# Performance work log

Hardware: AMD Instinct MI355X
Metric: run time of the kernel (lower is better)

The kernel has to match this reference:

```python
import jax, jax.numpy as jnp
import numpy as np

DIM = 4096
N_HEADS = 32
HEAD_DIM = DIM // N_HEADS
BSZ = 4
SEQLEN = 512
MAX_SEQ = 2048
NEG = -1e9


def _qlinear(x, q, s):
    # int-quantized weight [out,in] dequantized with per-output-channel scale
    w = q.astype(jnp.float32) * s[:, None]
    return jnp.einsum('bsd,od->bso', x, w)


def _apply_rotary(xq, xk, cos, sin):
    # xq,xk: [b,s,h,hd]; cos,sin: [s,hd/2]
    def rot(t):
        b, s, h, d = t.shape
        t = t.reshape(b, s, h, d // 2, 2)
        tr, ti = t[..., 0], t[..., 1]
        c = cos[None, :, None, :]
        sn = sin[None, :, None, :]
        out_r = tr * c - ti * sn
        out_i = tr * sn + ti * c
        return jnp.stack([out_r, out_i], axis=-1).reshape(b, s, h, d)
    return rot(xq), rot(xk)


def setup_inputs() -> dict:
    key = jax.random.key(0)
    ks = jax.random.split(key, 12)
    x = jax.random.normal(ks[0], (BSZ, SEQLEN, DIM), dtype=jnp.float32)
    inv = 1.0 / (10000.0 ** (jnp.arange(0, HEAD_DIM, 2, dtype=jnp.float32) / HEAD_DIM))
    ang = jnp.arange(SEQLEN, dtype=jnp.float32)[:, None] * inv[None, :]
    freqs_cos, freqs_sin = jnp.cos(ang), jnp.sin(ang)
    input_idexes = jnp.arange(SEQLEN, dtype=jnp.int32)  # cache slots being written
    # causal additive mask over full cache: query at position i may attend j <= i
    j = jnp.arange(MAX_SEQ)
    mask = jnp.where(j[None, :] <= input_idexes[:, None], 0.0, NEG).astype(jnp.float32)
    mask = mask[None, None]  # [1,1,S,MAX_SEQ]
    cache_k = jnp.zeros((BSZ, MAX_SEQ, N_HEADS, HEAD_DIM), jnp.float32)
    cache_v = jnp.zeros((BSZ, MAX_SEQ, N_HEADS, HEAD_DIM), jnp.float32)
    SCALE = 2.0 / (127.0 * np.sqrt(DIM))
    def mkw(kq, kscale):
        q = jax.random.randint(kq, (DIM, DIM), -127, 128, dtype=jnp.int32)
        s = jax.random.uniform(kscale, (DIM,), dtype=jnp.float32) * SCALE
        return q, s
    wq_q, wq_s = mkw(ks[1], ks[2])
    wk_q, wk_s = mkw(ks[3], ks[4])
    wv_q, wv_s = mkw(ks[5], ks[6])
    wo_q, wo_s = mkw(ks[7], ks[8])
    return dict(x=x, freqs_cos=freqs_cos, freqs_sin=freqs_sin, mask=mask,
                input_idexes=input_idexes, cache_k=cache_k, cache_v=cache_v,
                wq_q=wq_q, wq_s=wq_s, wk_q=wk_q, wk_s=wk_s,
                wv_q=wv_q, wv_s=wv_s, wo_q=wo_q, wo_s=wo_s)


def reference(x, freqs_cos, freqs_sin, mask, input_idexes, cache_k, cache_v,
              wq_q, wq_s, wk_q, wk_s, wv_q, wv_s, wo_q, wo_s):
    bsz, seqlen, _ = x.shape
    xq = _qlinear(x, wq_q, wq_s).reshape(bsz, seqlen, N_HEADS, HEAD_DIM)
    xk = _qlinear(x, wk_q, wk_s).reshape(bsz, seqlen, N_HEADS, HEAD_DIM)
    xv = _qlinear(x, wv_q, wv_s).reshape(bsz, seqlen, N_HEADS, HEAD_DIM)
    xq, xk = _apply_rotary(xq, xk, freqs_cos, freqs_sin)
    # KV-cache append (index_copy on dim 1)
    cache_k = cache_k.at[:, input_idexes].set(xk)
    cache_v = cache_v.at[:, input_idexes].set(xv)
    # [b,h,q,d] x [b,h,k,d] -> [b,h,q,k]
    scores = jnp.einsum('bqhd,bkhd->bhqk', xq, cache_k) / np.sqrt(HEAD_DIM)
    scores = scores + mask
    probs = jax.nn.softmax(scores.astype(jnp.float32), axis=-1).astype(xq.dtype)
    out = jnp.einsum('bhqk,bkhd->bqhd', probs, cache_v).reshape(bsz, seqlen, -1)
    out = _qlinear(out, wo_q, wo_s)
    return out, (cache_k, cache_v)
```

## Files before the change

kernel.cpp:

```cpp
#include <hip/hip_runtime.h>
#include <cstdint>
#include <cstddef>

typedef __bf16 bf16;
typedef __attribute__((ext_vector_type(8))) __bf16 bf16x8;
typedef __attribute__((ext_vector_type(2))) __bf16 bf16x2;
typedef __attribute__((ext_vector_type(4))) float f32x4;
typedef __attribute__((ext_vector_type(2))) float f32x2;
typedef __attribute__((ext_vector_type(4))) int i32x4;

#define DIMN 4096
#define SEQ 512
#define MAXSEQ 2048
#define NHEAD 32
#define HD 128

#define BM 128
#define BN 128
#define BK 32

__device__ __forceinline__ void gld_lds16(const void* g, void* l) {
  __builtin_amdgcn_global_load_lds(
      (const __attribute__((address_space(1))) unsigned int*)g,
      (__attribute__((address_space(3))) unsigned int*)l, 16, 0, 0);
}

__device__ __forceinline__ void gemm_core(const bf16* Ablk, const bf16* Bblk,
                                          int lda, int ldb, int kmax,
                                          f32x4 acc[4][4], bf16* As, bf16* Bs) {
  const int tid = threadIdx.x;
  const int wave = tid >> 6;
  const int lane = tid & 63;
  const int wm = (wave >> 1) * 64;
  const int wn = (wave & 1) * 64;
  const int lrow = lane & 15;
  const int lkq8 = (lane >> 4) * 8;
  const int srow = wave * 32 + (lane >> 2);
  const int scol = (lane & 3) * 8;
  const bf16* Ag = Ablk + (size_t)srow * lda + scol;
  const bf16* Bg = Bblk + (size_t)srow * ldb + scol;
  bf16* lA = As + wave * 32 * BK;
  bf16* lB = Bs + wave * 32 * BK;

  for (int k0 = 0; k0 < kmax; k0 += BK) {
    __syncthreads();
    gld_lds16(Ag + k0, lA);
    gld_lds16(Ag + k0 + (size_t)16 * lda, lA + 16 * BK);
    gld_lds16(Bg + k0, lB);
    gld_lds16(Bg + k0 + (size_t)16 * ldb, lB + 16 * BK);
    __syncthreads();
    bf16x8 a[4], b[4];
#pragma unroll
    for (int i = 0; i < 4; ++i)
      a[i] = *(const bf16x8*)(As + (wm + i * 16 + lrow) * BK + lkq8);
#pragma unroll
    for (int i = 0; i < 4; ++i)
      b[i] = *(const bf16x8*)(Bs + (wn + i * 16 + lrow) * BK + lkq8);
#pragma unroll
    for (int mi = 0; mi < 4; ++mi)
#pragma unroll
      for (int ni = 0; ni < 4; ++ni)
        acc[mi][ni] = __builtin_amdgcn_mfma_f32_16x16x32_bf16(a[mi], b[ni], acc[mi][ni], 0, 0, 0);
  }
}


#define PBAR do {                              \
    asm volatile("" ::: "memory");             \
    __builtin_amdgcn_sched_barrier(0);         \
    __builtin_amdgcn_s_barrier();              \
    __builtin_amdgcn_sched_barrier(0);         \
    asm volatile("" ::: "memory");             \
  } while (0)

#define STG_A(KT, C, LB) \
  gld_lds16(Asrc + (KT) * 128 + (size_t)(C) * 64 * DIMN, (LB) + (C) * 8192 + sdst)
#define STG_B(KT, C, LB) \
  gld_lds16(Bsrc + (KT) * 128 + (size_t)(C) * 64 * DIMN, (LB) + 16384 + (C) * 8192 + sdst)

#define LDA8(DST, MI, H, LB) \
  DST = *(const i32x4*)((LB) + (MI) * 2048 + aoff + ((H) ? g1off : g0off))
#define LDB8(DST, NI, H, LB) \
  DST = *(const i32x4*)((LB) + 16384 + (NI) * 2048 + boff + ((H) ? g1off : g0off))

#define MFMA16I()                                                           \
    __builtin_amdgcn_s_setprio(1);                                          \
    _Pragma("unroll") for (int _i = 0; _i < 4; ++_i)                        \
      _Pragma("unroll") for (int _n = 0; _n < 4; ++_n)                      \
        acc[_i][_n] = __builtin_amdgcn_mfma_i32_16x16x64_i8(                \
            a[_i], b[_n], acc[_i][_n], 0, 0, 0);                            \
    __builtin_amdgcn_s_setprio(0)

#define TILE3(T, CUR, STG) do {                                             \
    i32x4 a[4], b[4];                                                       \
                         \
    _Pragma("unroll") for (int n = 0; n < 4; ++n) LDB8(b[n], n, 0, CUR);    \
    _Pragma("unroll") for (int i = 0; i < 4; ++i) LDA8(a[i], i, 0, CUR);    \
    STG_B((T) + 2, 0, STG);                                                 \
    STG_B((T) + 2, 1, STG);                                                 \
    STG_A((T) + 2, 0, STG);                                                 \
    MFMA16I();                                                              \
                        \
    _Pragma("unroll") for (int n = 0; n < 4; ++n) LDB8(b[n], n, 1, CUR);    \
    _Pragma("unroll") for (int i = 0; i < 4; ++i) LDA8(a[i], i, 1, CUR);    \
    STG_B((T) + 2, 2, STG);                                                 \
    STG_B((T) + 2, 3, STG);                                                 \
    STG_A((T) + 2, 1, STG);                                                 \
    MFMA16I();                                                              \
                                   \
    asm volatile("s_waitcnt vmcnt(6)" ::: "memory");                        \
    __builtin_amdgcn_sched_barrier(0);                                      \
    __builtin_amdgcn_s_barrier();                                           \
    __builtin_amdgcn_sched_barrier(0);                                      \
  } while (0)

__device__ __forceinline__ void gemm128x256_i8(const char* __restrict__ Ablk,
                                               const char* __restrict__ Bblk,
                                               char* lds, i32x4 acc[4][4]) {
  const int tid = threadIdx.x;
  const int wave = tid >> 6, lane = tid & 63;
  const int wm = (wave >> 2) * 64, wn = (wave & 3) * 64;
  const int lrow = lane & 15, q = lane >> 4;
  const int qx = q ^ (lrow & 3);
  const int hbit = (lrow >> 2) & 1;
  const int g0off = (((hbit) << 2) | qx) << 4;
  const int g1off = (((hbit ^ 1) << 2) | qx) << 4;
  const int aoff = (wm + lrow) * 128;
  const int boff = (wn + lrow) * 128;
  const int gsw = ((lane & 7) ^ (lane >> 3)) << 4;
  const char* Asrc = Ablk + (size_t)(wave * 8 + (lane >> 3)) * DIMN + gsw;
  const char* Bsrc = Bblk + (size_t)(wave * 8 + (lane >> 3)) * DIMN + gsw;
  const int sdst = wave * 1024;
  char* const L0 = lds;
  char* const L1 = lds + 49152;
  char* const L2 = lds + 98304;

  STG_A(0, 0, L0); STG_A(0, 1, L0);
  STG_B(0, 0, L0); STG_B(0, 1, L0); STG_B(0, 2, L0); STG_B(0, 3, L0);
  STG_A(1, 0, L1); STG_A(1, 1, L1);
  STG_B(1, 0, L1); STG_B(1, 1, L1); STG_B(1, 2, L1); STG_B(1, 3, L1);
  asm volatile("s_waitcnt vmcnt(6)" ::: "memory");
  __builtin_amdgcn_sched_barrier(0);
  __builtin_amdgcn_s_barrier();
  __builtin_amdgcn_sched_barrier(0);

  for (int t = 0; t < 30; t += 3) {
    TILE3(t, L0, L2);
    TILE3(t + 1, L1, L0);
    TILE3(t + 2, L2, L1);
  }
  TILE3(30, L0, L2);
  TILE3(31, L1, L0);
}

#define ACC_INIT_F(acc)                                 \
  f32x4 acc[4][4];                                      \
  _Pragma("unroll") for (int _i = 0; _i < 4; ++_i)      \
      _Pragma("unroll") for (int _j = 0; _j < 4; ++_j)  \
          acc[_i][_j] = f32x4{0.f, 0.f, 0.f, 0.f};

#define ACC_INIT_I8(acc)                                \
  i32x4 acc[4][4];                                      \
  _Pragma("unroll") for (int _i = 0; _i < 4; ++_i)      \
      _Pragma("unroll") for (int _j = 0; _j < 4; ++_j)  \
          acc[_i][_j] = i32x4{0, 0, 0, 0};

#define EPI_COORDS                                      \
  const int lane = threadIdx.x & 63;                    \
  const int wave = threadIdx.x >> 6;                    \
  const int wm = (wave >> 1) * 64, wn = (wave & 1) * 64;\
  const int cq = (lane >> 4) * 4, cc = lane & 15;

#define EPI8_COORDS                                      \
  const int lane = threadIdx.x & 63;                     \
  const int wave = threadIdx.x >> 6;                     \
  const int wm = (wave >> 2) * 64, wn = (wave & 3) * 64; \
  const int cq = (lane >> 4) * 4, cc = lane & 15;

__global__ __launch_bounds__(256) void k_prep(
    const int* __restrict__ q0, const int* __restrict__ q1,
    const int* __restrict__ q2, const int* __restrict__ q3,
    char* __restrict__ w8, const float* __restrict__ x,
    char* __restrict__ x8, float* __restrict__ xs,
    float* __restrict__ ck, float* __restrict__ cv) {
  __shared__ float red[4];
  const int bx = blockIdx.x;
  const int tid = threadIdx.x;
  if (bx < 16384) {
    const int w = bx >> 12;
    const int* q = (w == 0) ? q0 : (w == 1) ? q1 : (w == 2) ? q2 : q3;
    char* wp = w8 + (size_t)w * 16777216ull;
    size_t i = ((size_t)(bx & 4095) * 256 + tid) * 16;
    const i32x4* qp = (const i32x4*)(q + i);
    i32x4 a = qp[0], b = qp[1], c = qp[2], d = qp[3];
    i32x4 o;
    o[0] = (a[0] & 255) | ((a[1] & 255) << 8) | ((a[2] & 255) << 16) | (a[3] << 24);
    o[1] = (b[0] & 255) | ((b[1] & 255) << 8) | ((b[2] & 255) << 16) | (b[3] << 24);
    o[2] = (c[0] & 255) | ((c[1] & 255) << 8) | ((c[2] & 255) << 16) | (c[3] << 24);
    o[3] = (d[0] & 255) | ((d[1] & 255) << 8) | ((d[2] & 255) << 16) | (d[3] << 24);
    *(i32x4*)(wp + i) = o;
  } else if (bx < 18432) {
    const int row = bx - 16384;
    const float* src = x + (size_t)row * DIMN + tid * 16;
    f32x4 v[4];
#pragma unroll
    for (int j = 0; j < 4; ++j) v[j] = ((const f32x4*)src)[j];
    float am = 0.f;
#pragma unroll
    for (int j = 0; j < 4; ++j)
#pragma unroll
      for (int e = 0; e < 4; ++e) am = fmaxf(am, fabsf(v[j][e]));
#pragma unroll
    for (int off = 32; off; off >>= 1) am = fmaxf(am, __shfl_xor(am, off, 64));
    if ((tid & 63) == 0) red[tid >> 6] = am;
    __syncthreads();
    am = fmaxf(fmaxf(red[0], red[1]), fmaxf(red[2], red[3]));
    const float inv = am > 0.f ? 127.f / am : 0.f;
    i32x4 o;
#pragma unroll
    for (int j = 0; j < 4; ++j) {
      int b0 = (int)rintf(v[j][0] * inv), b1 = (int)rintf(v[j][1] * inv);
      int b2 = (int)rintf(v[j][2] * inv), b3 = (int)rintf(v[j][3] * inv);
      o[j] = (b0 & 255) | ((b1 & 255) << 8) | ((b2 & 255) << 16) | (b3 << 24);
    }
    *(i32x4*)(x8 + (size_t)row * DIMN + tid * 16) = o;
    if (tid == 0) xs[row] = am * (1.f / 127.f);
  } else {
    const int z = bx - 18432;
    const int region = z / 6144;
    const int zoff = z - region * 6144;
    const int b = region >> 1;
    float* base = (region & 1) ? cv : ck;
    char* p = (char*)(base + ((size_t)b * MAXSEQ + SEQ) * DIMN);
    *(f32x4*)(p + (size_t)zoff * 4096 + tid * 16) = f32x4{0.f, 0.f, 0.f, 0.f};
  }
}

__global__ __launch_bounds__(256) void k_quant_attn(const bf16* __restrict__ at,
                                                    char* __restrict__ a8,
                                                    float* __restrict__ as_) {
  __shared__ float red[4];
  const int row = blockIdx.x, tid = threadIdx.x;
  const bf16* src = at + (size_t)row * DIMN + tid * 16;
  bf16x8 h0 = ((const bf16x8*)src)[0], h1 = ((const bf16x8*)src)[1];
  float f[16];
#pragma unroll
  for (int j = 0; j < 8; ++j) { f[j] = (float)h0[j]; f[8 + j] = (float)h1[j]; }
  float am = 0.f;
#pragma unroll
  for (int j = 0; j < 16; ++j) am = fmaxf(am, fabsf(f[j]));
#pragma unroll
  for (int off = 32; off; off >>= 1) am = fmaxf(am, __shfl_xor(am, off, 64));
  if ((tid & 63) == 0) red[tid >> 6] = am;
  __syncthreads();
  am = fmaxf(fmaxf(red[0], red[1]), fmaxf(red[2], red[3]));
  const float inv = am > 0.f ? 127.f / am : 0.f;
  i32x4 o;
#pragma unroll
  for (int j = 0; j < 4; ++j) {
    int b0 = (int)rintf(f[j * 4 + 0] * inv), b1 = (int)rintf(f[j * 4 + 1] * inv);
    int b2 = (int)rintf(f[j * 4 + 2] * inv), b3 = (int)rintf(f[j * 4 + 3] * inv);
    o[j] = (b0 & 255) | ((b1 & 255) << 8) | ((b2 & 255) << 16) | (b3 << 24);
  }
  *(i32x4*)(a8 + (size_t)row * DIMN + tid * 16) = o;
  if (tid == 0) as_[row] = am * (1.f / 127.f);
}

__global__ __launch_bounds__(512, 2) void k_gemm_qkv8(
    const char* __restrict__ X8, const char* __restrict__ W8,
    const float* __restrict__ xs, const float* __restrict__ sq,
    const float* __restrict__ sk, const float* __restrict__ sv,
    const float* __restrict__ fc, const float* __restrict__ fs,
    const int* __restrict__ idx, bf16* __restrict__ qbf,
    bf16* __restrict__ kbf, float* __restrict__ ck, float* __restrict__ cv) {
  __shared__ __align__(16) char lds[147456];
  const int n0 = blockIdx.x * 256;
  const int m0 = blockIdx.y * 128;
  const int z = blockIdx.z;
  const char* W = W8 + (size_t)z * 16777216ull;
  const float* sw = (z == 0) ? sq : (z == 1) ? sk : sv;
  ACC_INIT_I8(acc);
  gemm128x256_i8(X8 + (size_t)m0 * DIMN, W + (size_t)n0 * DIMN, lds, acc);
  EPI8_COORDS;
  if (z < 2) {
    bf16* dst = (z == 0) ? qbf : kbf;
#pragma unroll
    for (int mi = 0; mi < 4; ++mi)
#pragma unroll
      for (int ni = 0; ni < 4; ++ni)
#pragma unroll
        for (int r = 0; r < 4; ++r) {
          const int row = m0 + wm + mi * 16 + cq + r;
          const int col = n0 + wn + ni * 16 + cc;
          const float v = (float)acc[mi][ni][r] * xs[row] * sw[col];
          const float pv = __shfl_xor(v, 1, 64);
          const int s = row & 511, b = row >> 9;
          const int hd = col & 127, h = col >> 7;
          const int d2 = hd >> 1;
          const float c = fc[s * 64 + d2], sn = fs[s * 64 + d2];
          const float o = (col & 1) ? (pv * sn + v * c) : (v * c - pv * sn);
          dst[(((size_t)(b * NHEAD + h)) * SEQ + s) * HD + hd] = (bf16)o;
          if (z == 1) {
            const int pos = idx[s];
            ck[((size_t)b * MAXSEQ + pos) * DIMN + col] = o;
          }
        }
  } else {
#pragma unroll
    for (int mi = 0; mi < 4; ++mi)
#pragma unroll
      for (int ni = 0; ni < 4; ++ni)
#pragma unroll
        for (int r = 0; r < 4; ++r) {
          const int row = m0 + wm + mi * 16 + cq + r;
          const int col = n0 + wn + ni * 16 + cc;
          const int s = row & 511, b = row >> 9;
          cv[((size_t)b * MAXSEQ + s) * DIMN + col] =
              (float)acc[mi][ni][r] * xs[row] * sw[col];
        }
  }
}

__global__ __launch_bounds__(256) void k_vt(const float* __restrict__ cv,
                                            bf16* __restrict__ vt) {
  __shared__ float tile[32][129];
  const int s0 = blockIdx.x * 32;
  const int bh = blockIdx.y;
  const int b = bh >> 5, h = bh & 31;
  const int tid = threadIdx.x;
  const float* src = cv + (size_t)b * MAXSEQ * DIMN + h * HD;
#pragma unroll
  for (int p = 0; p < 16; ++p) {
    const int row = p * 2 + (tid >> 7);
    const int d = tid & 127;
    tile[row][d] = src[(size_t)(s0 + row) * DIMN + d];
  }
  __syncthreads();
  bf16* dst = vt + (size_t)bh * HD * SEQ;
#pragma unroll
  for (int c = 0; c < 16; ++c) {
    const int d = c * 8 + (tid >> 5);
    const int sl = tid & 31;
    dst[(size_t)d * SEQ + s0 + sl] = (bf16)tile[sl][d];
  }
}

__constant__ int g_tm[10] = {0, 1, 1, 2, 2, 2, 3, 3, 3, 3};
__constant__ int g_tn[10] = {0, 0, 1, 0, 1, 2, 0, 1, 2, 3};

__global__ __launch_bounds__(256, 2) void k_gemm_qk(
    const bf16* __restrict__ qb, const bf16* __restrict__ kb,
    bf16* __restrict__ sc) {
  const int m0 = g_tm[blockIdx.x] * BM;
  const int n0 = g_tn[blockIdx.x] * BN;
  const int bh = blockIdx.z;
  __shared__ __align__(16) bf16 As[BM * BK];
  __shared__ __align__(16) bf16 Bs[BN * BK];
  ACC_INIT_F(acc);
  gemm_core(qb + (size_t)bh * SEQ * HD + (size_t)m0 * HD,
            kb + (size_t)bh * SEQ * HD + (size_t)n0 * HD, HD, HD, HD, acc, As, Bs);
  EPI_COORDS;
  bf16* dst = sc + (size_t)bh * SEQ * SEQ;
#pragma unroll
  for (int mi = 0; mi < 4; ++mi)
#pragma unroll
    for (int ni = 0; ni < 4; ++ni)
#pragma unroll
      for (int r = 0; r < 4; ++r) {
        const int row = m0 + wm + mi * 16 + cq + r;
        const int col = n0 + wn + ni * 16 + cc;
        dst[(size_t)row * SEQ + col] = (bf16)(acc[mi][ni][r] * 0.08838834764831845f);
      }
}

__global__ __launch_bounds__(256) void k_softmax(bf16* __restrict__ sc) {
  const int row = blockIdx.x * 4 + (threadIdx.x >> 6);
  const int lane = threadIdx.x & 63;
  const int q = row & 511;
  bf16* p = sc + (size_t)row * SEQ + lane * 8;
  bf16x8 v8 = *(const bf16x8*)p;
  float lv[8];
  float m = -3.0e38f;
#pragma unroll
  for (int j = 0; j < 8; ++j) {
    const int kj = lane * 8 + j;
    lv[j] = (kj <= q) ? (float)v8[j] : -3.0e38f;
    m = fmaxf(m, lv[j]);
  }
#pragma unroll
  for (int off = 32; off; off >>= 1) m = fmaxf(m, __shfl_xor(m, off, 64));
  float e[8];
  float sum = 0.f;
#pragma unroll
  for (int j = 0; j < 8; ++j) {
    e[j] = (lane * 8 + j <= q) ? __expf(lv[j] - m) : 0.f;
    sum += e[j];
  }
#pragma unroll
  for (int off = 32; off; off >>= 1) sum += __shfl_xor(sum, off, 64);
  const float r = 1.f / sum;
  bf16x8 o;
#pragma unroll
  for (int j = 0; j < 8; ++j) o[j] = (bf16)(e[j] * r);
  *(bf16x8*)p = o;
}

__global__ __launch_bounds__(256, 2) void k_gemm_pv(
    const bf16* __restrict__ P, const bf16* __restrict__ vt,
    bf16* __restrict__ attn) {
  const int m0 = blockIdx.y * BM;
  const int bh = blockIdx.z;
  const int kmax = m0 + BM;
  __shared__ __align__(16) bf16 As[BM * BK];
  __shared__ __align__(16) bf16 Bs[BN * BK];
  ACC_INIT_F(acc);
  gemm_core(P + (size_t)bh * SEQ * SEQ + (size_t)m0 * SEQ,
            vt + (size_t)bh * HD * SEQ, SEQ, SEQ, kmax, acc, As, Bs);
  EPI_COORDS;
  const int b = bh >> 5, h = bh & 31;
#pragma unroll
  for (int mi = 0; mi < 4; ++mi)
#pragma unroll
    for (int ni = 0; ni < 4; ++ni)
#pragma unroll
      for (int r = 0; r < 4; ++r) {
        const int row = m0 + wm + mi * 16 + cq + r;
        const int col = wn + ni * 16 + cc;
        attn[((size_t)(b * SEQ + row)) * DIMN + h * HD + col] = (bf16)acc[mi][ni][r];
      }
}

__global__ __launch_bounds__(512, 2) void k_gemm_out8(
    const char* __restrict__ A8, const char* __restrict__ WO8,
    const float* __restrict__ as_, const float* __restrict__ so,
    float* __restrict__ out) {
  __shared__ __align__(16) char lds[147456];
  const int n0 = blockIdx.x * 256;
  const int m0 = blockIdx.y * 128;
  ACC_INIT_I8(acc);
  gemm128x256_i8(A8 + (size_t)m0 * DIMN, WO8 + (size_t)n0 * DIMN, lds, acc);
  EPI8_COORDS;
#pragma unroll
  for (int mi = 0; mi < 4; ++mi)
#pragma unroll
    for (int ni = 0; ni < 4; ++ni)
#pragma unroll
      for (int r = 0; r < 4; ++r) {
        const int row = m0 + wm + mi * 16 + cq + r;
        const int col = n0 + wn + ni * 16 + cc;
        out[(size_t)row * DIMN + col] = (float)acc[mi][ni][r] * as_[row] * so[col];
      }
}

extern "C" void kernel_launch(void* const* d_in, const int* in_sizes, int n_in,
                              void* d_out, int out_size, void* d_ws, size_t ws_size,
                              hipStream_t stream) {
  const float* x = (const float*)d_in[0];
  const float* fc = (const float*)d_in[1];
  const float* fs = (const float*)d_in[2];
  const int* idx = (const int*)d_in[4];
  const int* wq_q = (const int*)d_in[7];
  const int* wk_q = (const int*)d_in[9];
  const int* wv_q = (const int*)d_in[11];
  const int* wo_q = (const int*)d_in[13];
  const float* wq_s = (const float*)d_in[8];
  const float* wk_s = (const float*)d_in[10];
  const float* wv_s = (const float*)d_in[12];
  const float* wo_s = (const float*)d_in[14];

  float* out = (float*)d_out;
  float* ck_out = out + 8388608;
  float* cv_out = ck_out + 33554432;

  char* ws = (char*)d_ws;
  char* W8   = ws;
  char* X8   = ws + 67108864ull;
  float* XS  = (float*)(ws + 75497472ull);
  float* AS  = (float*)(ws + 75513856ull);
  bf16* QBF  = (bf16*)(ws + 83886080ull);
  bf16* KBF  = (bf16*)(ws + 100663296ull);
  bf16* VTB  = (bf16*)(ws + 117440512ull);
  bf16* ATTN = (bf16*)(ws + 134217728ull);
  char* A8   = ws + 150994944ull;
  bf16* SC   = (bf16*)(ws + 167772160ull);

  k_prep<<<dim3(67584), 256, 0, stream>>>(wq_q, wk_q, wv_q, wo_q, W8, x, X8, XS,
                                          ck_out, cv_out);
  k_gemm_qkv8<<<dim3(16, 16, 3), 512, 0, stream>>>(
      X8, W8, XS, wq_s, wk_s, wv_s, fc, fs, idx, QBF, KBF, ck_out, cv_out);
  k_vt<<<dim3(16, 128), 256, 0, stream>>>(cv_out, VTB);
  k_gemm_qk<<<dim3(10, 1, 128), 256, 0, stream>>>(QBF, KBF, SC);
  k_softmax<<<dim3(16384), 256, 0, stream>>>(SC);
  k_gemm_pv<<<dim3(1, 4, 128), 256, 0, stream>>>(SC, VTB, ATTN);
  k_quant_attn<<<dim3(2048), 256, 0, stream>>>(ATTN, A8, AS);
  k_gemm_out8<<<dim3(16, 16), 512, 0, stream>>>(A8, W8 + 50331648ull, AS, wo_s, out);
  (void)in_sizes; (void)n_in; (void)out_size; (void)ws_size;
}
```

Baseline: 857.0 us.

## Move KV-cache tail zeroing from prep kernel into QKV GEMM main loop

The prep kernel no longer zeroes the unused tail of the KV caches. Instead, each QKV GEMM block writes a slice of zeros once per K-loop iteration, interleaved with the MFMA pipeline. The goal is to hide this write-only memory traffic, about 200MB, behind the compute-bound int8 GEMM and to shrink the prep launch. In exchange it adds global stores inside the GEMM hot loop, which can compete with the operand loads and the vmcnt accounting.

```diff
diff --git a/kernel.cpp b/kernel.cpp
--- a/kernel.cpp
+++ b/kernel.cpp
@@ -112,11 +112,15 @@
     __builtin_amdgcn_sched_barrier(0);                                      \
     __builtin_amdgcn_s_barrier();                                           \
     __builtin_amdgcn_sched_barrier(0);                                      \
+     \
+    if (zp) *(f32x4*)(zp + ((size_t)(T) * 512 + tid) * 16) =                \
+        f32x4{0.f, 0.f, 0.f, 0.f};                                          \
   } while (0)
 
 __device__ __forceinline__ void gemm128x256_i8(const char* __restrict__ Ablk,
                                                const char* __restrict__ Bblk,
-                                               char* lds, i32x4 acc[4][4]) {
+                                               char* lds, i32x4 acc[4][4],
+                                               char* zp) {
   const int tid = threadIdx.x;
   const int wave = tid >> 6, lane = tid & 63;
   const int wm = (wave >> 2) * 64, wn = (wave & 3) * 64;
@@ -181,8 +185,7 @@
     const int* __restrict__ q0, const int* __restrict__ q1,
     const int* __restrict__ q2, const int* __restrict__ q3,
     char* __restrict__ w8, const float* __restrict__ x,
-    char* __restrict__ x8, float* __restrict__ xs,
-    float* __restrict__ ck, float* __restrict__ cv) {
+    char* __restrict__ x8, float* __restrict__ xs) {
   __shared__ float red[4];
   const int bx = blockIdx.x;
   const int tid = threadIdx.x;
@@ -199,7 +202,7 @@
     o[2] = (c[0] & 255) | ((c[1] & 255) << 8) | ((c[2] & 255) << 16) | (c[3] << 24);
     o[3] = (d[0] & 255) | ((d[1] & 255) << 8) | ((d[2] & 255) << 16) | (d[3] << 24);
     *(i32x4*)(wp + i) = o;
-  } else if (bx < 18432) {
+  } else {
     const int row = bx - 16384;
     const float* src = x + (size_t)row * DIMN + tid * 16;
     f32x4 v[4];
@@ -225,14 +228,6 @@
     }
     *(i32x4*)(x8 + (size_t)row * DIMN + tid * 16) = o;
     if (tid == 0) xs[row] = am * (1.f / 127.f);
-  } else {
-    const int z = bx - 18432;
-    const int region = z / 6144;
-    const int zoff = z - region * 6144;
-    const int b = region >> 1;
-    float* base = (region & 1) ? cv : ck;
-    char* p = (char*)(base + ((size_t)b * MAXSEQ + SEQ) * DIMN);
-    *(f32x4*)(p + (size_t)zoff * 4096 + tid * 16) = f32x4{0.f, 0.f, 0.f, 0.f};
   }
 }
 
@@ -279,8 +274,13 @@
   const int z = blockIdx.z;
   const char* W = W8 + (size_t)z * 16777216ull;
   const float* sw = (z == 0) ? sq : (z == 1) ? sk : sv;
+  const int g = z * 256 + blockIdx.y * 16 + blockIdx.x;
+  const int zr = g / 96, zo = g % 96;
+  float* zbase = ((zr & 1) ? cv : ck) +
+                 ((size_t)(zr >> 1) * MAXSEQ + SEQ) * DIMN;
+  char* zp = (char*)zbase + (size_t)zo * 262144ull;
   ACC_INIT_I8(acc);
-  gemm128x256_i8(X8 + (size_t)m0 * DIMN, W + (size_t)n0 * DIMN, lds, acc);
+  gemm128x256_i8(X8 + (size_t)m0 * DIMN, W + (size_t)n0 * DIMN, lds, acc, zp);
   EPI8_COORDS;
   if (z < 2) {
     bf16* dst = (z == 0) ? qbf : kbf;
@@ -438,7 +438,8 @@
   const int n0 = blockIdx.x * 256;
   const int m0 = blockIdx.y * 128;
   ACC_INIT_I8(acc);
-  gemm128x256_i8(A8 + (size_t)m0 * DIMN, WO8 + (size_t)n0 * DIMN, lds, acc);
+  gemm128x256_i8(A8 + (size_t)m0 * DIMN, WO8 + (size_t)n0 * DIMN, lds, acc,
+                 nullptr);
   EPI8_COORDS;
 #pragma unroll
   for (int mi = 0; mi < 4; ++mi)
@@ -484,8 +485,7 @@
   char* A8   = ws + 150994944ull;
   bf16* SC   = (bf16*)(ws + 167772160ull);
 
-  k_prep<<<dim3(67584), 256, 0, stream>>>(wq_q, wk_q, wv_q, wo_q, W8, x, X8, XS,
-                                          ck_out, cv_out);
+  k_prep<<<dim3(18432), 256, 0, stream>>>(wq_q, wk_q, wv_q, wo_q, W8, x, X8, XS);
   k_gemm_qkv8<<<dim3(16, 16, 3), 512, 0, stream>>>(
       X8, W8, XS, wq_s, wk_s, wv_s, fc, fs, idx, QBF, KBF, ck_out, cv_out);
   k_vt<<<dim3(16, 128), 256, 0, stream>>>(cv_out, VTB);
```

After: 866.8 us. No clear change (+1.1%).
